# Kernel optimization log

Hardware: AMD Instinct MI355X
Metric: run time of the kernel (lower is better)

Reference implementation:

```python
import jax, jax.numpy as jnp
import numpy as np

EPS = 1e-5  # BatchNorm eps


def _conv_bn_tanh(h, w, b, g, be, m, v):
    # 3x3 conv, stride 1, SAME padding (pad = k//2), NCHW / OIHW
    y = jax.lax.conv_general_dilated(
        h, w, window_strides=(1, 1), padding='SAME',
        dimension_numbers=('NCHW', 'OIHW', 'NCHW'))
    y = y + b[None, :, None, None]
    # BatchNorm inference: gamma * (y - mean) / sqrt(var + eps) + beta
    scale = g * jax.lax.rsqrt(v + EPS)
    y = y * scale[None, :, None, None] + (be - m * scale)[None, :, None, None]
    return jnp.tanh(y)


def _unfold3x3(x):
    # torch F.unfold(k=3, pad=1, stride=1) -> (N, C, 9, H, W), kernel positions row-major
    N, C, H, W = x.shape
    xp = jnp.pad(x, ((0, 0), (0, 0), (1, 1), (1, 1)))
    patches = [xp[:, :, i:i + H, j:j + W] for i in range(3) for j in range(3)]
    return jnp.stack(patches, axis=2)  # (N, C, 9, H, W)


def setup_inputs() -> dict:
    key = jax.random.key(0)
    ks = jax.random.split(key, 24)
    N, C, H, W = 8, 64, 128, 128
    INTER, FEAT, NB, KK = 64, 6, 6, 9
    d = {}
    d['x'] = jax.random.normal(ks[0], (N, C, H, W), jnp.float32)
    d['w0'] = jax.random.normal(ks[1], (INTER, C, 3, 3), jnp.float32) * 0.05
    d['b0'] = jax.random.normal(ks[2], (INTER,), jnp.float32) * 0.05
    d['g0'] = jax.random.uniform(ks[3], (INTER,), jnp.float32)
    d['be0'] = jax.random.normal(ks[4], (INTER,), jnp.float32) * 0.05
    d['m0'] = jax.random.normal(ks[5], (INTER,), jnp.float32) * 0.05
    d['v0'] = jax.random.uniform(ks[6], (INTER,), jnp.float32)
    d['wm'] = jax.random.normal(ks[7], (5, INTER, INTER, 3, 3), jnp.float32) * 0.05
    d['bm'] = jax.random.normal(ks[8], (5, INTER), jnp.float32) * 0.05
    d['gm'] = jax.random.uniform(ks[9], (5, INTER), jnp.float32)
    d['bem'] = jax.random.normal(ks[10], (5, INTER), jnp.float32) * 0.05
    d['mm'] = jax.random.normal(ks[11], (5, INTER), jnp.float32) * 0.05
    d['vm'] = jax.random.uniform(ks[12], (5, INTER), jnp.float32)
    OC = FEAT * NB  # 36
    d['wl'] = jax.random.normal(ks[13], (OC, INTER, 3, 3), jnp.float32) * 0.05
    d['bl'] = jax.random.normal(ks[14], (OC,), jnp.float32) * 0.05
    d['gl'] = jax.random.uniform(ks[15], (OC,), jnp.float32)
    d['bel'] = jax.random.normal(ks[16], (OC,), jnp.float32) * 0.05
    d['ml'] = jax.random.normal(ks[17], (OC,), jnp.float32) * 0.05
    d['vl'] = jax.random.uniform(ks[18], (OC,), jnp.float32)
    d['bases'] = jax.random.normal(ks[19], (NB, KK), jnp.float32)  # FB bases buffer (6, 9)
    return d


def reference(x, w0, b0, g0, be0, m0, v0, wm, bm, gm, bem, mm, vm,
              wl, bl, gl, bel, ml, vl, bases):
    N, C, H, W = x.shape
    FEAT, NB = 6, 6
    # bases_net: conv-bn-tanh x7 (eval mode, dropout no-ops)
    h = _conv_bn_tanh(x, w0, b0, g0, be0, m0, v0)
    for i in range(5):
        h = _conv_bn_tanh(h, wm[i], bm[i], gm[i], bem[i], mm[i], vm[i])
    h = _conv_bn_tanh(h, wl, bl, gl, bel, ml, vl)  # (N, 36, H, W)
    bfeat = h.reshape(N, FEAT, NB, H, W)
    # per-pixel basis coefficients: (N, M, 9, H, W)
    bcoef = jnp.einsum('bmkhw,kl->bmlhw', bfeat, bases)
    patches = _unfold3x3(x)  # (N, C, 9, H, W)
    # dynamic conv: combine per-pixel coeffs with unfolded input
    out = jnp.einsum('bmlhw,bclhw->bcmhw', bcoef, patches)  # (N, C, M, H, W)
    return out.reshape(N, C * NB, H, W)
```

## Files before the change

### kernel.cpp

```cpp
#include <hip/hip_runtime.h>
#include <hip/hip_bf16.h>

typedef short bf16x4 __attribute__((ext_vector_type(4)));
typedef short bf16x8 __attribute__((ext_vector_type(8)));
typedef float f32x4  __attribute__((ext_vector_type(4)));

__device__ inline unsigned short f2us(float f) {
    __hip_bfloat16 h = __float2bfloat16(f);
    return *(unsigned short*)&h;
}
__device__ inline float us2f(unsigned short u) {
    union { unsigned int i; float f; } c; c.i = ((unsigned int)u) << 16; return c.f;
}
__device__ inline float tanh_fast(float x) {
    float xs = fminf(fmaxf(x, -20.f), 20.f);
    float t = __expf(2.f * xs);
    return 1.f - 2.f / (t + 1.f);
}

__device__ inline void gload_lds16(const void* g, void* l) {
    __builtin_amdgcn_global_load_lds(
        (const __attribute__((address_space(1))) void*)g,
        (__attribute__((address_space(3))) void*)l,
        16, 0, 0);
}

__global__ __launch_bounds__(256) void prep_x(const float* __restrict__ x,
                                              unsigned short* __restrict__ xcl)
{
    __shared__ unsigned short t2[128 * 68];
    int bid = blockIdx.x;
    int n = bid >> 7, h = bid & 127;
    const float* xp = x + (size_t)n * 64 * 16384 + h * 128;
    int t = threadIdx.x;
    for (int i = t; i < 8192; i += 256) {
        int ci = i >> 7, w = i & 127;
        t2[w * 68 + ci] = f2us(xp[(size_t)ci * 16384 + w]);
    }
    __syncthreads();
    unsigned short* op = xcl + ((size_t)(n * 16384 + h * 128)) * 64;
    for (int i = t; i < 1024; i += 256) {
        int w = i >> 3, c8 = i & 7;
        union { bf16x4 v[2]; uint4 q; } u;
        u.v[0] = *(bf16x4*)&t2[w * 68 + c8 * 8];
        u.v[1] = *(bf16x4*)&t2[w * 68 + c8 * 8 + 4];
        *(uint4*)(op + w * 64 + c8 * 8) = u.q;
    }
}

__global__ void prep_wf(const float* __restrict__ w0, const float* __restrict__ wm,
                        const float* __restrict__ wl, unsigned short* __restrict__ Wf)
{
    int idx = blockIdx.x * 256 + threadIdx.x;
    if (idx >= 258048) return;
    int l = idx / 36864, r = idx - l * 36864;
    int tp = r >> 12, r2 = r & 4095;
    int hh = r2 >> 11, nb = (r2 >> 9) & 3, ln = (r2 >> 3) & 63, j = r2 & 7;
    int ci = hh * 32 + (ln >> 4) * 8 + j;
    int co = nb * 16 + (ln & 15);
    float val = 0.f;
    if (l < 6) {
        const float* src = (l == 0) ? w0 : (wm + (size_t)(l - 1) * 36864);
        val = src[(co * 64 + ci) * 9 + tp];
    } else if (co < 36) {
        val = wl[(co * 64 + ci) * 9 + tp];
    }
    Wf[idx] = f2us(val);
}

__global__ void prep_ab(const float* b0, const float* g0, const float* be0,
                        const float* m0, const float* v0,
                        const float* bm, const float* gm, const float* bem,
                        const float* mm, const float* vm,
                        const float* bl, const float* gl, const float* bel,
                        const float* ml, const float* vl,
                        float* __restrict__ Af, float* __restrict__ Bf)
{
    int idx = blockIdx.x * 256 + threadIdx.x;
    if (idx >= 448) return;
    int l = idx >> 6, c = idx & 63;
    float b, g, be, m, v;
    if (l == 0) {
        b = b0[c]; g = g0[c]; be = be0[c]; m = m0[c]; v = v0[c];
    } else if (l < 6) {
        int o = (l - 1) * 64 + c;
        b = bm[o]; g = gm[o]; be = bem[o]; m = mm[o]; v = vm[o];
    } else {
        if (c >= 36) { Af[idx] = 0.f; Bf[idx] = 0.f; return; }
        b = bl[c]; g = gl[c]; be = bel[c]; m = ml[c]; v = vl[c];
    }
    float s = g / sqrtf(v + 1e-5f);
    Af[idx] = s;
    Bf[idx] = (b - m) * s + be;
}

#define LDS_W_OFF 78336
__global__ __launch_bounds__(512, 2)
void conv_mfma(const unsigned short* __restrict__ src,
               const unsigned short* __restrict__ Wf,
               const float* __restrict__ A, const float* __restrict__ B,
               unsigned short* __restrict__ dst)
{
    __shared__ __align__(16) unsigned char smem[152064];
    const int n = blockIdx.z;
    const int h0 = blockIdx.y * 16, w0 = blockIdx.x * 32;
    const int t = threadIdx.x;
    const int ln = t & 63, wv = t >> 6;
    const int xln = ln & 15, qd = ln >> 4;
    const size_t ibase = (size_t)n * 16384 * 64;

    {
        uint4 z = make_uint4(0u, 0u, 0u, 0u);
        for (int c = t; c < 4896; c += 512)
            *(uint4*)(smem + (size_t)c * 16) = z;
    }
    __syncthreads();

    const unsigned short* srcn = src + ibase;
    for (int i = wv; i < 77; i += 8) {
        int g = i * 64 + ln;
        int p = g >> 3, jj = g & 7;
        int ty = (p * 1928) >> 16;
        int tx = p - ty * 34;
        int gy = h0 + ty - 1, gx = w0 + tx - 1;
        int js = jj ^ (p & 7);
        bool ok = (g < 4896) & ((unsigned)gy < 128u) & ((unsigned)gx < 128u);
        const unsigned short* gsrc = srcn + (ptrdiff_t)(gy * 128 + gx) * 64 + js * 8;
        if (ok) gload_lds16(gsrc, smem + (size_t)i * 1024);
    }
    for (int i = wv; i < 72; i += 8) {
        const unsigned short* gsrc = Wf + ((size_t)(i * 64 + ln)) * 8;
        gload_lds16(gsrc, smem + LDS_W_OFF + (size_t)i * 1024);
    }
    __syncthreads();

    f32x4 acc[2][2][4];
#pragma unroll
    for (int rh = 0; rh < 2; ++rh)
#pragma unroll
        for (int hf = 0; hf < 2; ++hf)
#pragma unroll
            for (int nb = 0; nb < 4; ++nb)
                acc[rh][hf][nb] = (f32x4){0.f, 0.f, 0.f, 0.f};

    const int rbase = wv * 2;
#pragma unroll
    for (int tp = 0; tp < 9; ++tp) {
        const int ky = tp / 3, kx = tp % 3;
        bf16x8 b[2][4];
#pragma unroll
        for (int hh = 0; hh < 2; ++hh)
#pragma unroll
            for (int nb = 0; nb < 4; ++nb)
                b[hh][nb] = *(const bf16x8*)(smem + LDS_W_OFF +
                    (((((tp * 2 + hh) * 4 + nb) * 64) + ln) << 4));
#pragma unroll
        for (int rh = 0; rh < 2; ++rh) {
#pragma unroll
            for (int hf = 0; hf < 2; ++hf) {
                const int p = (rbase + rh + ky) * 34 + hf * 16 + xln + kx;
                const int pb = p * 128, sw = (p & 7) << 4;
#pragma unroll
                for (int hh = 0; hh < 2; ++hh) {
                    bf16x8 a = *(const bf16x8*)(smem + pb +
                                                (((qd + 4 * hh) << 4) ^ sw));
#pragma unroll
                    for (int nb = 0; nb < 4; ++nb)
                        acc[rh][hf][nb] = __builtin_amdgcn_mfma_f32_16x16x32_bf16(
                            a, b[hh][nb], acc[rh][hf][nb], 0, 0, 0);
                }
            }
        }
    }

#pragma unroll
    for (int nb = 0; nb < 4; ++nb) {
        const int co = nb * 16 + xln;
        const float As = A[co], Bs = B[co];
#pragma unroll
        for (int rh = 0; rh < 2; ++rh) {
            const int gy = h0 + rbase + rh;
            unsigned short* dp = dst + ibase + (size_t)(gy * 128) * 64;
#pragma unroll
            for (int hf = 0; hf < 2; ++hf) {
#pragma unroll
                for (int r = 0; r < 4; ++r) {
                    const int gx = w0 + hf * 16 + qd * 4 + r;
                    float y = tanh_fast(fmaf(acc[rh][hf][nb][r], As, Bs));
                    dp[(size_t)gx * 64 + co] = f2us(y);
                }
            }
        }
    }
}

__global__ __launch_bounds__(256)
void dyn_conv(const float* __restrict__ x, const unsigned short* __restrict__ h7,
              const float* __restrict__ bases, float* __restrict__ out)
{
    __shared__ float tile[32 * 10 * 34];
    const int n = blockIdx.z;
    const int h0 = blockIdx.y * 8, w0 = blockIdx.x * 32;
    const float* xp = x + (size_t)n * 64 * 16384;
    const int t = threadIdx.x;
    const int tw = t & 31, th = t >> 5;
    const int h = h0 + th, w = w0 + tw;

    float bs[54];
#pragma unroll
    for (int i = 0; i < 54; ++i) bs[i] = bases[i];

    union { uint4 q[5]; unsigned short s[40]; } hv;
    const unsigned short* hp = h7 + (size_t)(n * 16384 + h * 128 + w) * 64;
#pragma unroll
    for (int i = 0; i < 5; ++i) hv.q[i] = ((const uint4*)hp)[i];

    float coef[54];
#pragma unroll
    for (int i = 0; i < 54; ++i) coef[i] = 0.f;
#pragma unroll
    for (int m = 0; m < 6; ++m)
#pragma unroll
        for (int k = 0; k < 6; ++k) {
            float f = us2f(hv.s[m * 6 + k]);
#pragma unroll
            for (int l = 0; l < 9; ++l)
                coef[m * 9 + l] = fmaf(f, bs[k * 9 + l], coef[m * 9 + l]);
        }

    float* op = out + (size_t)n * 384 * 16384 + h * 128 + w;

    for (int half = 0; half < 2; ++half) {
        if (half) __syncthreads();
        for (int idx = t; idx < 32 * 340; idx += 256) {
            int ci = idx / 340, r = idx % 340, y = r / 34, xw = r % 34;
            int gy = h0 + y - 1, gx = w0 + xw - 1;
            float v = 0.f;
            if ((unsigned)gy < 128u && (unsigned)gx < 128u)
                v = xp[(size_t)(half * 32 + ci) * 16384 + gy * 128 + gx];
            tile[idx] = v;
        }
        __syncthreads();

#pragma unroll 1
        for (int c = 0; c < 32; ++c) {
            float xv[9];
#pragma unroll
            for (int ky = 0; ky < 3; ++ky)
#pragma unroll
                for (int kx = 0; kx < 3; ++kx)
                    xv[ky * 3 + kx] = tile[c * 340 + (th + ky) * 34 + (tw + kx)];
            int cg = half * 32 + c;
#pragma unroll
            for (int m = 0; m < 6; ++m) {
                float s = 0.f;
#pragma unroll
                for (int l = 0; l < 9; ++l) s = fmaf(coef[m * 9 + l], xv[l], s);
                op[(size_t)(cg * 6 + m) * 16384] = s;
            }
        }
    }
}

extern "C" void kernel_launch(void* const* d_in, const int* in_sizes, int n_in,
                              void* d_out, int out_size, void* d_ws, size_t ws_size,
                              hipStream_t stream)
{
    const float* x   = (const float*)d_in[0];
    const float* w0  = (const float*)d_in[1];
    const float* b0  = (const float*)d_in[2];
    const float* g0  = (const float*)d_in[3];
    const float* be0 = (const float*)d_in[4];
    const float* m0  = (const float*)d_in[5];
    const float* v0  = (const float*)d_in[6];
    const float* wm  = (const float*)d_in[7];
    const float* bm  = (const float*)d_in[8];
    const float* gm  = (const float*)d_in[9];
    const float* bem = (const float*)d_in[10];
    const float* mm  = (const float*)d_in[11];
    const float* vm  = (const float*)d_in[12];
    const float* wl  = (const float*)d_in[13];
    const float* bl  = (const float*)d_in[14];
    const float* gl  = (const float*)d_in[15];
    const float* bel = (const float*)d_in[16];
    const float* ml  = (const float*)d_in[17];
    const float* vl  = (const float*)d_in[18];
    const float* bas = (const float*)d_in[19];

    unsigned short* Wfb = (unsigned short*)d_ws;
    float* Af  = (float*)((char*)d_ws + 524288);
    float* Bf  = Af + 448;
    unsigned short* xcl  = (unsigned short*)((char*)d_ws + (size_t)(2  << 20));
    unsigned short* bufA = (unsigned short*)((char*)d_ws + (size_t)(2  << 20) + 16777216);
    unsigned short* bufB = (unsigned short*)((char*)d_ws + (size_t)(2  << 20) + 2 * 16777216);

    prep_x<<<1024, 256, 0, stream>>>(x, xcl);
    prep_wf<<<1008, 256, 0, stream>>>(w0, wm, wl, Wfb);
    prep_ab<<<2, 256, 0, stream>>>(b0, g0, be0, m0, v0,
                                   bm, gm, bem, mm, vm,
                                   bl, gl, bel, ml, vl, Af, Bf);

    dim3 cg(4, 8, 8);
    conv_mfma<<<cg, 512, 0, stream>>>(xcl,  Wfb + 0 * 36864, Af + 0,   Bf + 0,   bufA);
    conv_mfma<<<cg, 512, 0, stream>>>(bufA, Wfb + 1 * 36864, Af + 64,  Bf + 64,  bufB);
    conv_mfma<<<cg, 512, 0, stream>>>(bufB, Wfb + 2 * 36864, Af + 128, Bf + 128, bufA);
    conv_mfma<<<cg, 512, 0, stream>>>(bufA, Wfb + 3 * 36864, Af + 192, Bf + 192, bufB);
    conv_mfma<<<cg, 512, 0, stream>>>(bufB, Wfb + 4 * 36864, Af + 256, Bf + 256, bufA);
    conv_mfma<<<cg, 512, 0, stream>>>(bufA, Wfb + 5 * 36864, Af + 320, Bf + 320, bufB);
    conv_mfma<<<cg, 512, 0, stream>>>(bufB, Wfb + 6 * 36864, Af + 384, Bf + 384, bufA);

    dim3 dg(4, 16, 8);
    dyn_conv<<<dg, 256, 0, stream>>>(x, bufA, bas, (float*)d_out);
}
```

Baseline: 413.2 us.

## Merge prep kernels, drop LDS zero-fill via zero page, vectorize conv stores

Fuses the three preprocessing kernels into one launch and adds a small zeroed global buffer. Out-of-bounds halo loads now read from that buffer instead of relying on an LDS zero-fill pass and barrier. The weight layout permutes output channels so each lane owns four consecutive channels, which allows 8-byte ushort4 stores in the epilogue instead of scalar 2-byte stores. The cost is a trickier index mapping that must stay consistent between the weight prep and the conv epilogue.

```diff
diff --git a/kernel.cpp b/kernel.cpp
--- a/kernel.cpp
+++ b/kernel.cpp
@@ -25,73 +25,76 @@
         16, 0, 0);
 }
 
-__global__ __launch_bounds__(256) void prep_x(const float* __restrict__ x,
-                                              unsigned short* __restrict__ xcl)
+__global__ __launch_bounds__(256)
+void prep_all(const float* __restrict__ x, unsigned short* __restrict__ xcl,
+              const float* __restrict__ w0, const float* __restrict__ wm,
+              const float* __restrict__ wl, unsigned short* __restrict__ Wf,
+              const float* b0, const float* g0, const float* be0,
+              const float* m0, const float* v0,
+              const float* bm, const float* gm, const float* bem,
+              const float* mm, const float* vm,
+              const float* bl, const float* gl, const float* bel,
+              const float* ml, const float* vl,
+              float* __restrict__ Af, float* __restrict__ Bf,
+              unsigned int* __restrict__ zp)
 {
-    __shared__ unsigned short t2[128 * 68];
-    int bid = blockIdx.x;
-    int n = bid >> 7, h = bid & 127;
-    const float* xp = x + (size_t)n * 64 * 16384 + h * 128;
-    int t = threadIdx.x;
-    for (int i = t; i < 8192; i += 256) {
-        int ci = i >> 7, w = i & 127;
-        t2[w * 68 + ci] = f2us(xp[(size_t)ci * 16384 + w]);
-    }
-    __syncthreads();
-    unsigned short* op = xcl + ((size_t)(n * 16384 + h * 128)) * 64;
-    for (int i = t; i < 1024; i += 256) {
-        int w = i >> 3, c8 = i & 7;
-        union { bf16x4 v[2]; uint4 q; } u;
-        u.v[0] = *(bf16x4*)&t2[w * 68 + c8 * 8];
-        u.v[1] = *(bf16x4*)&t2[w * 68 + c8 * 8 + 4];
-        *(uint4*)(op + w * 64 + c8 * 8) = u.q;
-    }
-}
-
-__global__ void prep_wf(const float* __restrict__ w0, const float* __restrict__ wm,
-                        const float* __restrict__ wl, unsigned short* __restrict__ Wf)
-{
-    int idx = blockIdx.x * 256 + threadIdx.x;
-    if (idx >= 258048) return;
-    int l = idx / 36864, r = idx - l * 36864;
-    int tp = r >> 12, r2 = r & 4095;
-    int hh = r2 >> 11, nb = (r2 >> 9) & 3, ln = (r2 >> 3) & 63, j = r2 & 7;
-    int ci = hh * 32 + (ln >> 4) * 8 + j;
-    int co = nb * 16 + (ln & 15);
-    float val = 0.f;
-    if (l < 6) {
-        const float* src = (l == 0) ? w0 : (wm + (size_t)(l - 1) * 36864);
-        val = src[(co * 64 + ci) * 9 + tp];
-    } else if (co < 36) {
-        val = wl[(co * 64 + ci) * 9 + tp];
-    }
-    Wf[idx] = f2us(val);
-}
-
-__global__ void prep_ab(const float* b0, const float* g0, const float* be0,
-                        const float* m0, const float* v0,
-                        const float* bm, const float* gm, const float* bem,
-                        const float* mm, const float* vm,
-                        const float* bl, const float* gl, const float* bel,
-                        const float* ml, const float* vl,
-                        float* __restrict__ Af, float* __restrict__ Bf)
-{
-    int idx = blockIdx.x * 256 + threadIdx.x;
-    if (idx >= 448) return;
-    int l = idx >> 6, c = idx & 63;
-    float b, g, be, m, v;
-    if (l == 0) {
-        b = b0[c]; g = g0[c]; be = be0[c]; m = m0[c]; v = v0[c];
-    } else if (l < 6) {
-        int o = (l - 1) * 64 + c;
-        b = bm[o]; g = gm[o]; be = bem[o]; m = mm[o]; v = vm[o];
+    const int bid = blockIdx.x;
+    const int t = threadIdx.x;
+    if (bid < 1024) {
+        __shared__ unsigned short t2[128 * 68];
+        int n = bid >> 7, h = bid & 127;
+        const float* xp = x + (size_t)n * 64 * 16384 + h * 128;
+        for (int i = t; i < 8192; i += 256) {
+            int ci = i >> 7, w = i & 127;
+            t2[w * 68 + ci] = f2us(xp[(size_t)ci * 16384 + w]);
+        }
+        __syncthreads();
+        unsigned short* op = xcl + ((size_t)(n * 16384 + h * 128)) * 64;
+        for (int i = t; i < 1024; i += 256) {
+            int w = i >> 3, c8 = i & 7;
+            union { bf16x4 v[2]; uint4 q; } u;
+            u.v[0] = *(bf16x4*)&t2[w * 68 + c8 * 8];
+            u.v[1] = *(bf16x4*)&t2[w * 68 + c8 * 8 + 4];
+            *(uint4*)(op + w * 64 + c8 * 8) = u.q;
+        }
+    } else if (bid < 2032) {
+        int idx = (bid - 1024) * 256 + t;
+        int l = idx / 36864, r = idx - l * 36864;
+        int tp = r >> 12, r2 = r & 4095;
+        int hh = r2 >> 11, nb = (r2 >> 9) & 3, ln = (r2 >> 3) & 63, j = r2 & 7;
+        int ci = hh * 32 + (ln >> 4) * 8 + j;
+        int co = (ln & 15) * 4 + nb;
+        float val = 0.f;
+        if (l < 6) {
+            const float* src = (l == 0) ? w0 : (wm + (size_t)(l - 1) * 36864);
+            val = src[(co * 64 + ci) * 9 + tp];
+        } else if (co < 36) {
+            val = wl[(co * 64 + ci) * 9 + tp];
+        }
+        Wf[idx] = f2us(val);
     } else {
-        if (c >= 36) { Af[idx] = 0.f; Bf[idx] = 0.f; return; }
-        b = bl[c]; g = gl[c]; be = bel[c]; m = ml[c]; v = vl[c];
-    }
-    float s = g / sqrtf(v + 1e-5f);
-    Af[idx] = s;
-    Bf[idx] = (b - m) * s + be;
+        int idx = (bid - 2032) * 256 + t;
+        if (bid == 2033 && t >= 192) zp[t - 192] = 0u;
+        if (idx < 448) {
+            int l = idx >> 6, c = idx & 63;
+            float b, g, be, m, v;
+            bool zero = false;
+            if (l == 0) {
+                b = b0[c]; g = g0[c]; be = be0[c]; m = m0[c]; v = v0[c];
+            } else if (l < 6) {
+                int o = (l - 1) * 64 + c;
+                b = bm[o]; g = gm[o]; be = bem[o]; m = mm[o]; v = vm[o];
+            } else if (c < 36) {
+                b = bl[c]; g = gl[c]; be = bel[c]; m = ml[c]; v = vl[c];
+            } else zero = true;
+            if (zero) { Af[idx] = 0.f; Bf[idx] = 0.f; }
+            else {
+                float s = g / sqrtf(v + 1e-5f);
+                Af[idx] = s;
+                Bf[idx] = (b - m) * s + be;
+            }
+        }
+    }
 }
 
 #define LDS_W_OFF 78336
@@ -99,7 +102,8 @@
 void conv_mfma(const unsigned short* __restrict__ src,
                const unsigned short* __restrict__ Wf,
                const float* __restrict__ A, const float* __restrict__ B,
-               unsigned short* __restrict__ dst)
+               unsigned short* __restrict__ dst,
+               const unsigned short* __restrict__ zp)
 {
     __shared__ __align__(16) unsigned char smem[152064];
     const int n = blockIdx.z;
@@ -109,13 +113,6 @@
     const int xln = ln & 15, qd = ln >> 4;
     const size_t ibase = (size_t)n * 16384 * 64;
 
-    {
-        uint4 z = make_uint4(0u, 0u, 0u, 0u);
-        for (int c = t; c < 4896; c += 512)
-            *(uint4*)(smem + (size_t)c * 16) = z;
-    }
-    __syncthreads();
-
     const unsigned short* srcn = src + ibase;
     for (int i = wv; i < 77; i += 8) {
         int g = i * 64 + ln;
@@ -124,9 +121,11 @@
         int tx = p - ty * 34;
         int gy = h0 + ty - 1, gx = w0 + tx - 1;
         int js = jj ^ (p & 7);
-        bool ok = (g < 4896) & ((unsigned)gy < 128u) & ((unsigned)gx < 128u);
-        const unsigned short* gsrc = srcn + (ptrdiff_t)(gy * 128 + gx) * 64 + js * 8;
-        if (ok) gload_lds16(gsrc, smem + (size_t)i * 1024);
+        const unsigned short* gsrc =
+            (((unsigned)gy < 128u) & ((unsigned)gx < 128u))
+                ? srcn + (ptrdiff_t)(gy * 128 + gx) * 64 + js * 8
+                : zp;
+        if (g < 4896) gload_lds16(gsrc, smem + (size_t)i * 1024);
     }
     for (int i = wv; i < 72; i += 8) {
         const unsigned short* gsrc = Wf + ((size_t)(i * 64 + ln)) * 8;
@@ -173,22 +172,23 @@
         }
     }
 
-#pragma unroll
-    for (int nb = 0; nb < 4; ++nb) {
-        const int co = nb * 16 + xln;
-        const float As = A[co], Bs = B[co];
-#pragma unroll
-        for (int rh = 0; rh < 2; ++rh) {
-            const int gy = h0 + rbase + rh;
-            unsigned short* dp = dst + ibase + (size_t)(gy * 128) * 64;
-#pragma unroll
-            for (int hf = 0; hf < 2; ++hf) {
-#pragma unroll
-                for (int r = 0; r < 4; ++r) {
-                    const int gx = w0 + hf * 16 + qd * 4 + r;
-                    float y = tanh_fast(fmaf(acc[rh][hf][nb][r], As, Bs));
-                    dp[(size_t)gx * 64 + co] = f2us(y);
-                }
+    const float4 A4 = *(const float4*)&A[xln * 4];
+    const float4 B4 = *(const float4*)&B[xln * 4];
+#pragma unroll
+    for (int rh = 0; rh < 2; ++rh) {
+        const int gy = h0 + rbase + rh;
+        unsigned short* dp = dst + ibase + (size_t)(gy * 128) * 64 + xln * 4;
+#pragma unroll
+        for (int hf = 0; hf < 2; ++hf) {
+#pragma unroll
+            for (int r = 0; r < 4; ++r) {
+                const int gx = w0 + hf * 16 + qd * 4 + r;
+                ushort4 o;
+                o.x = f2us(tanh_fast(fmaf(acc[rh][hf][0][r], A4.x, B4.x)));
+                o.y = f2us(tanh_fast(fmaf(acc[rh][hf][1][r], A4.y, B4.y)));
+                o.z = f2us(tanh_fast(fmaf(acc[rh][hf][2][r], A4.z, B4.z)));
+                o.w = f2us(tanh_fast(fmaf(acc[rh][hf][3][r], A4.w, B4.w)));
+                *(ushort4*)(dp + (size_t)gx * 64) = o;
             }
         }
     }
@@ -290,24 +290,25 @@
     unsigned short* Wfb = (unsigned short*)d_ws;
     float* Af  = (float*)((char*)d_ws + 524288);
     float* Bf  = Af + 448;
+    unsigned int* zp = (unsigned int*)((char*)d_ws + (1 << 20));
     unsigned short* xcl  = (unsigned short*)((char*)d_ws + (size_t)(2  << 20));
     unsigned short* bufA = (unsigned short*)((char*)d_ws + (size_t)(2  << 20) + 16777216);
     unsigned short* bufB = (unsigned short*)((char*)d_ws + (size_t)(2  << 20) + 2 * 16777216);
 
-    prep_x<<<1024, 256, 0, stream>>>(x, xcl);
-    prep_wf<<<1008, 256, 0, stream>>>(w0, wm, wl, Wfb);
-    prep_ab<<<2, 256, 0, stream>>>(b0, g0, be0, m0, v0,
-                                   bm, gm, bem, mm, vm,
-                                   bl, gl, bel, ml, vl, Af, Bf);
+    prep_all<<<2034, 256, 0, stream>>>(x, xcl, w0, wm, wl, Wfb,
+                                       b0, g0, be0, m0, v0,
+                                       bm, gm, bem, mm, vm,
+                                       bl, gl, bel, ml, vl, Af, Bf, zp);
 
     dim3 cg(4, 8, 8);
-    conv_mfma<<<cg, 512, 0, stream>>>(xcl,  Wfb + 0 * 36864, Af + 0,   Bf + 0,   bufA);
-    conv_mfma<<<cg, 512, 0, stream>>>(bufA, Wfb + 1 * 36864, Af + 64,  Bf + 64,  bufB);
-    conv_mfma<<<cg, 512, 0, stream>>>(bufB, Wfb + 2 * 36864, Af + 128, Bf + 128, bufA);
-    conv_mfma<<<cg, 512, 0, stream>>>(bufA, Wfb + 3 * 36864, Af + 192, Bf + 192, bufB);
-    conv_mfma<<<cg, 512, 0, stream>>>(bufB, Wfb + 4 * 36864, Af + 256, Bf + 256, bufA);
-    conv_mfma<<<cg, 512, 0, stream>>>(bufA, Wfb + 5 * 36864, Af + 320, Bf + 320, bufB);
-    conv_mfma<<<cg, 512, 0, stream>>>(bufB, Wfb + 6 * 36864, Af + 384, Bf + 384, bufA);
+    const unsigned short* zps = (const unsigned short*)zp;
+    conv_mfma<<<cg, 512, 0, stream>>>(xcl,  Wfb + 0 * 36864, Af + 0,   Bf + 0,   bufA, zps);
+    conv_mfma<<<cg, 512, 0, stream>>>(bufA, Wfb + 1 * 36864, Af + 64,  Bf + 64,  bufB, zps);
+    conv_mfma<<<cg, 512, 0, stream>>>(bufB, Wfb + 2 * 36864, Af + 128, Bf + 128, bufA, zps);
+    conv_mfma<<<cg, 512, 0, stream>>>(bufA, Wfb + 3 * 36864, Af + 192, Bf + 192, bufB, zps);
+    conv_mfma<<<cg, 512, 0, stream>>>(bufB, Wfb + 4 * 36864, Af + 256, Bf + 256, bufA, zps);
+    conv_mfma<<<cg, 512, 0, stream>>>(bufA, Wfb + 5 * 36864, Af + 320, Bf + 320, bufB, zps);
+    conv_mfma<<<cg, 512, 0, stream>>>(bufB, Wfb + 6 * 36864, Af + 384, Bf + 384, bufA, zps);
 
     dim3 dg(4, 16, 8);
     dyn_conv<<<dg, 256, 0, stream>>>(x, bufA, bas, (float*)d_out);
```

After: 403.7 us. 2.3% less time.
